# Kernel optimization log

Hardware: AMD Instinct MI355X
Metric: run time of the kernel (lower is better)

Reference implementation:

```python
import jax, jax.numpy as jnp
import numpy as np

T, D, E, K = 8192, 4096, 64, 8


def setup_inputs() -> dict:
    key = jax.random.key(0)
    k1, k2, k3, k4 = jax.random.split(key, 4)
    x = jax.random.normal(k1, (T, D), dtype=jnp.float32)
    # nn.Linear stores weight as [out_features, in_features]
    Wg = jax.random.normal(k2, (E, D), dtype=jnp.float32) * (1.0 / np.sqrt(D))
    Wc = jax.random.normal(k3, (E, D), dtype=jnp.float32) * (1.0 / np.sqrt(D))
    extra_scale = jnp.zeros((E,), dtype=jnp.float32)  # init zeros as in module
    extra_bias = jax.random.normal(k4, (E,), dtype=jnp.float32) * 0.01
    return {"x": x, "Wg": Wg, "Wc": Wc, "extra_scale": extra_scale,
            "extra_bias": extra_bias, "topk": K}


def reference(x, Wg, Wc, extra_scale, extra_bias, topk):
    # scores = |classifier(x) * silu(gate(x))|, softmax in fp32
    gate = jnp.einsum('td,ed->te', x, Wg)        # [T, E]
    cls = jnp.einsum('td,ed->te', x, Wc)         # [T, E]
    scores = jnp.abs(cls * jax.nn.silu(gate))
    scores = jax.nn.softmax(scores.astype(jnp.float32), axis=-1)
    biased = scores + extra_bias[None, :]        # load-balance bias, used only for selection
    _, indices = jax.lax.top_k(biased, topk)     # [T, K]
    original = 1.0 + scores * extra_scale[None, :]
    weights = jnp.take_along_axis(original, indices, axis=1)  # [T, K]
    return weights.astype(x.dtype), indices
```

## Files before the change

### kernel.cpp

```cpp
#include <hip/hip_runtime.h>
#include <math.h>


#define T_DIM 8192
#define D_DIM 4096
#define E_DIM 64
#define N2    128
#define KTOP  8
#define MB_ROWS 128

typedef __attribute__((ext_vector_type(8)))  short bfrag8;
typedef __attribute__((ext_vector_type(16))) float f32x16;

__device__ __forceinline__ unsigned short f2bf_rne(float f) {
    unsigned int u = __float_as_uint(f);
    unsigned int r = u + 0x7fffu + ((u >> 16) & 1u);
    return (unsigned short)(r >> 16);
}
__device__ __forceinline__ float bf2f(unsigned short h) {
    return __uint_as_float(((unsigned int)h) << 16);
}
__device__ __forceinline__ void split3(float v, unsigned short& h,
                                       unsigned short& m, unsigned short& l) {
    h = f2bf_rne(v);
    const float r1 = v - bf2f(h);
    m = f2bf_rne(r1);
    const float r2 = r1 - bf2f(m);
    l = f2bf_rne(r2);
}

__global__ __launch_bounds__(256)
void router_prep(const float* __restrict__ Wg, const float* __restrict__ Wc,
                 unsigned short* __restrict__ Whi, unsigned short* __restrict__ Wmid,
                 unsigned short* __restrict__ Wlo)
{
    const int i   = blockIdx.x * 256 + threadIdx.x;
    const int row = i >> 10;
    const float* src = (row < E_DIM) ? (Wg + (size_t)row * D_DIM)
                                     : (Wc + (size_t)(row - E_DIM) * D_DIM);
    const float4 w = ((const float4*)src)[i & 1023];
    const float v[4] = {w.x, w.y, w.z, w.w};
    ushort4 hv, mv, lv;
    split3(v[0], hv.x, mv.x, lv.x);
    split3(v[1], hv.y, mv.y, lv.y);
    split3(v[2], hv.z, mv.z, lv.z);
    split3(v[3], hv.w, mv.w, lv.w);
    *(ushort4*)(Whi  + (size_t)i * 4) = hv;
    *(ushort4*)(Wmid + (size_t)i * 4) = mv;
    *(ushort4*)(Wlo  + (size_t)i * 4) = lv;
}

__global__ __launch_bounds__(256, 2)
void router_gemm(const float* __restrict__ x,
                 const unsigned short* __restrict__ Whi,
                 const unsigned short* __restrict__ Wmid,
                 const unsigned short* __restrict__ Wlo,
                 float* __restrict__ P,
                 int sliceK)
{
    const int tid  = threadIdx.x;
    const int lane = tid & 63;
    const int wid  = tid >> 6;
    const int l31  = lane & 31;
    const int lh   = lane >> 5;
    const int mb   = blockIdx.x;
    const int ks   = blockIdx.y;
    const int k0   = ks * sliceK;
    const int kend = k0 + sliceK;
    const int row0 = mb * MB_ROWS + wid * 32;

    f32x16 acc[4];
    #pragma unroll
    for (int n = 0; n < 4; ++n)
        #pragma unroll
        for (int r = 0; r < 16; ++r)
            acc[n][r] = 0.f;

    const float* xr = x + (size_t)(row0 + l31) * D_DIM;

    const float* xp0 = xr + k0 + lh * 8;
    float4 a00 = *(const float4*)(xp0);
    float4 a01 = *(const float4*)(xp0 + 4);
    float4 a10 = *(const float4*)(xp0 + 16);
    float4 a11 = *(const float4*)(xp0 + 20);

    for (int kk = k0; kk < kend; kk += 32) {
        bfrag8 ah[2], am[2], al[2];
        {
            const float av0[8] = {a00.x,a00.y,a00.z,a00.w,a01.x,a01.y,a01.z,a01.w};
            const float av1[8] = {a10.x,a10.y,a10.z,a10.w,a11.x,a11.y,a11.z,a11.w};
            #pragma unroll
            for (int j = 0; j < 8; ++j) {
                unsigned short h, m, l;
                split3(av0[j], h, m, l);
                ah[0][j] = (short)h; am[0][j] = (short)m; al[0][j] = (short)l;
                split3(av1[j], h, m, l);
                ah[1][j] = (short)h; am[1][j] = (short)m; al[1][j] = (short)l;
            }
        }

        if (kk + 32 < kend) {
            const float* xp = xr + (kk + 32) + lh * 8;
            a00 = *(const float4*)(xp);
            a01 = *(const float4*)(xp + 4);
            a10 = *(const float4*)(xp + 16);
            a11 = *(const float4*)(xp + 20);
        }

        #pragma unroll
        for (int n = 0; n < 4; ++n) {
            #pragma unroll
            for (int h2 = 0; h2 < 2; ++h2) {
                const size_t bo = (size_t)(n * 32 + l31) * D_DIM + kk + h2 * 16 + lh * 8;
                const bfrag8 bh = *(const bfrag8*)(Whi  + bo);
                const bfrag8 bm = *(const bfrag8*)(Wmid + bo);
                const bfrag8 bl = *(const bfrag8*)(Wlo  + bo);
                acc[n] = __builtin_amdgcn_mfma_f32_32x32x16_bf16(ah[h2], bl, acc[n], 0, 0, 0);
                acc[n] = __builtin_amdgcn_mfma_f32_32x32x16_bf16(al[h2], bh, acc[n], 0, 0, 0);
                acc[n] = __builtin_amdgcn_mfma_f32_32x32x16_bf16(am[h2], bm, acc[n], 0, 0, 0);
                acc[n] = __builtin_amdgcn_mfma_f32_32x32x16_bf16(ah[h2], bm, acc[n], 0, 0, 0);
                acc[n] = __builtin_amdgcn_mfma_f32_32x32x16_bf16(am[h2], bh, acc[n], 0, 0, 0);
                acc[n] = __builtin_amdgcn_mfma_f32_32x32x16_bf16(ah[h2], bh, acc[n], 0, 0, 0);
            }
        }
    }

    float* Pb = P + ((size_t)ks * T_DIM + row0) * N2 + l31;
    #pragma unroll
    for (int n = 0; n < 4; ++n)
        #pragma unroll
        for (int r = 0; r < 16; ++r) {
            const int wrow = (r & 3) + 8 * (r >> 2) + 4 * lh;
            Pb[(size_t)wrow * N2 + n * 32] = acc[n][r];
        }
}

__global__ __launch_bounds__(256)
void router_topk(const float* __restrict__ P,
                 const float* __restrict__ scale,
                 const float* __restrict__ bias,
                 float* __restrict__ out,
                 int ksplit)
{
    const int lane = threadIdx.x & 63;
    const int wid  = threadIdx.x >> 6;
    const int row  = blockIdx.x * 4 + wid;

    float g = 0.f, c = 0.f;
    for (int ks = 0; ks < ksplit; ++ks) {
        const float* p = P + ((size_t)ks * T_DIM + row) * N2;
        g += p[lane];
        c += p[E_DIM + lane];
    }
    const float sg = g / (1.f + expf(-g));
    const float v  = fabsf(c * sg);

    float m = v;
    #pragma unroll
    for (int off = 32; off >= 1; off >>= 1) m = fmaxf(m, __shfl_xor(m, off));
    const float e = expf(v - m);
    float Z = e;
    #pragma unroll
    for (int off = 32; off >= 1; off >>= 1) Z += __shfl_xor(Z, off);
    const float s = e / Z;

    const float sc  = scale[lane];
    float cur = s + bias[lane];

    float myw = 0.f; int myi = 0;
    #pragma unroll
    for (int j = 0; j < KTOP; ++j) {
        float bv = cur; int bi = lane;
        #pragma unroll
        for (int off = 32; off >= 1; off >>= 1) {
            const float ov = __shfl_xor(bv, off);
            const int   oi = __shfl_xor(bi, off);
            if (ov > bv || (ov == bv && oi < bi)) { bv = ov; bi = oi; }
        }
        const float s_bi  = __shfl(s,  bi);
        const float sc_bi = __shfl(sc, bi);
        const float w = 1.f + s_bi * sc_bi;
        if (lane == j)  { myw = w; myi = bi; }
        if (lane == bi) cur = -INFINITY;
    }

    if (lane < KTOP) {
        out[(size_t)row * KTOP + lane] = myw;
        out[(size_t)T_DIM * KTOP + (size_t)row * KTOP + lane] = (float)myi;
    }
}

extern "C" void kernel_launch(void* const* d_in, const int* in_sizes, int n_in,
                              void* d_out, int out_size, void* d_ws, size_t ws_size,
                              hipStream_t stream)
{
    const float* x  = (const float*)d_in[0];
    const float* Wg = (const float*)d_in[1];
    const float* Wc = (const float*)d_in[2];
    const float* sc = (const float*)d_in[3];
    const float* bs = (const float*)d_in[4];
    float* out = (float*)d_out;
    float* P   = (float*)d_ws;

    const size_t PER = (size_t)T_DIM * N2 * sizeof(float);
    const size_t WSP = (size_t)N2 * D_DIM * sizeof(unsigned short);

    int S = 8;
    while (S > 1 && (size_t)S * PER + 3 * WSP > ws_size) S >>= 1;
    const int sliceK = D_DIM / S;

    unsigned short* Whi  = (unsigned short*)((char*)d_ws + (size_t)S * PER);
    unsigned short* Wmid = Whi + (size_t)N2 * D_DIM;
    unsigned short* Wlo  = Wmid + (size_t)N2 * D_DIM;

    router_prep<<<512, 256, 0, stream>>>(Wg, Wc, Whi, Wmid, Wlo);
    router_gemm<<<dim3(T_DIM / MB_ROWS, S), 256, 0, stream>>>(x, Whi, Wmid, Wlo, P, sliceK);
    router_topk<<<T_DIM / 4, 256, 0, stream>>>(P, sc, bs, out, S);
}
```

Baseline: 303.7 us.

## Split GEMM warps 2x2 over rows and columns with double-buffered A/B register prefetch

Changes the block tile from 128 rows with each warp covering all 128 output columns to 64 rows with a 2x2 warp grid, each warp covering 32 rows by 64 columns. This halves the accumulators per warp and doubles the grid size. The K loop is unrolled by two and uses ping-pong register sets, so both the x fragments and the three bf16 weight fragments for the next step are loaded while the current MFMAs run. The goal is to hide global-load latency and raise occupancy. In exchange, each x row is now read by two warps, and the extra prefetch buffers add register pressure.

```diff
diff --git a/kernel.cpp b/kernel.cpp
--- a/kernel.cpp
+++ b/kernel.cpp
@@ -7,7 +7,7 @@
 #define E_DIM 64
 #define N2    128
 #define KTOP  8
-#define MB_ROWS 128
+#define MB_ROWS 64
 
 typedef __attribute__((ext_vector_type(8)))  short bfrag8;
 typedef __attribute__((ext_vector_type(16))) float f32x16;
@@ -50,6 +50,68 @@
     *(ushort4*)(Wlo  + (size_t)i * 4) = lv;
 }
 
+struct ASet { float4 c[4]; };
+struct BSet { bfrag8 h[4], m[4], l[4]; };
+
+__device__ __forceinline__ void loadA(ASet& A, const float* __restrict__ xr, int kk, int lh)
+{
+    const float* p = xr + kk + lh * 8;
+    A.c[0] = *(const float4*)(p);
+    A.c[1] = *(const float4*)(p + 4);
+    A.c[2] = *(const float4*)(p + 16);
+    A.c[3] = *(const float4*)(p + 20);
+}
+
+__device__ __forceinline__ void loadB(BSet& B,
+                                      const unsigned short* __restrict__ Whi,
+                                      const unsigned short* __restrict__ Wmid,
+                                      const unsigned short* __restrict__ Wlo,
+                                      size_t base )
+{
+    #pragma unroll
+    for (int n = 0; n < 2; ++n)
+        #pragma unroll
+        for (int h2 = 0; h2 < 2; ++h2) {
+            const size_t off = base + (size_t)n * 32 * D_DIM + h2 * 16;
+            B.h[n * 2 + h2] = *(const bfrag8*)(Whi  + off);
+            B.m[n * 2 + h2] = *(const bfrag8*)(Wmid + off);
+            B.l[n * 2 + h2] = *(const bfrag8*)(Wlo  + off);
+        }
+}
+
+__device__ __forceinline__ void splitA(const ASet& A, bfrag8 ah[2], bfrag8 am[2], bfrag8 al[2])
+{
+    #pragma unroll
+    for (int h2 = 0; h2 < 2; ++h2) {
+        const float4 q0 = A.c[h2 * 2], q1 = A.c[h2 * 2 + 1];
+        const float f[8] = {q0.x, q0.y, q0.z, q0.w, q1.x, q1.y, q1.z, q1.w};
+        #pragma unroll
+        for (int j = 0; j < 8; ++j) {
+            unsigned short h, m, l;
+            split3(f[j], h, m, l);
+            ah[h2][j] = (short)h; am[h2][j] = (short)m; al[h2][j] = (short)l;
+        }
+    }
+}
+
+__device__ __forceinline__ void mfmaStep(f32x16 acc[2], const bfrag8 ah[2],
+                                         const bfrag8 am[2], const bfrag8 al[2],
+                                         const BSet& B)
+{
+    #pragma unroll
+    for (int n = 0; n < 2; ++n)
+        #pragma unroll
+        for (int h2 = 0; h2 < 2; ++h2) {
+            const int q = n * 2 + h2;
+            acc[n] = __builtin_amdgcn_mfma_f32_32x32x16_bf16(ah[h2], B.l[q], acc[n], 0, 0, 0);
+            acc[n] = __builtin_amdgcn_mfma_f32_32x32x16_bf16(al[h2], B.h[q], acc[n], 0, 0, 0);
+            acc[n] = __builtin_amdgcn_mfma_f32_32x32x16_bf16(am[h2], B.m[q], acc[n], 0, 0, 0);
+            acc[n] = __builtin_amdgcn_mfma_f32_32x32x16_bf16(ah[h2], B.m[q], acc[n], 0, 0, 0);
+            acc[n] = __builtin_amdgcn_mfma_f32_32x32x16_bf16(am[h2], B.h[q], acc[n], 0, 0, 0);
+            acc[n] = __builtin_amdgcn_mfma_f32_32x32x16_bf16(ah[h2], B.h[q], acc[n], 0, 0, 0);
+        }
+}
+
 __global__ __launch_bounds__(256, 2)
 void router_gemm(const float* __restrict__ x,
                  const unsigned short* __restrict__ Whi,
@@ -61,73 +123,53 @@
     const int tid  = threadIdx.x;
     const int lane = tid & 63;
     const int wid  = tid >> 6;
+    const int wr   = wid >> 1;
+    const int wc   = wid & 1;
     const int l31  = lane & 31;
     const int lh   = lane >> 5;
     const int mb   = blockIdx.x;
     const int ks   = blockIdx.y;
     const int k0   = ks * sliceK;
     const int kend = k0 + sliceK;
-    const int row0 = mb * MB_ROWS + wid * 32;
-
-    f32x16 acc[4];
-    #pragma unroll
-    for (int n = 0; n < 4; ++n)
+    const int row0 = mb * MB_ROWS + wr * 32;
+    const int nbase = wc * 64;
+
+    f32x16 acc[2];
+    #pragma unroll
+    for (int n = 0; n < 2; ++n)
         #pragma unroll
         for (int r = 0; r < 16; ++r)
             acc[n][r] = 0.f;
 
     const float* xr = x + (size_t)(row0 + l31) * D_DIM;
-
-    const float* xp0 = xr + k0 + lh * 8;
-    float4 a00 = *(const float4*)(xp0);
-    float4 a01 = *(const float4*)(xp0 + 4);
-    float4 a10 = *(const float4*)(xp0 + 16);
-    float4 a11 = *(const float4*)(xp0 + 20);
-
-    for (int kk = k0; kk < kend; kk += 32) {
-        bfrag8 ah[2], am[2], al[2];
-        {
-            const float av0[8] = {a00.x,a00.y,a00.z,a00.w,a01.x,a01.y,a01.z,a01.w};
-            const float av1[8] = {a10.x,a10.y,a10.z,a10.w,a11.x,a11.y,a11.z,a11.w};
-            #pragma unroll
-            for (int j = 0; j < 8; ++j) {
-                unsigned short h, m, l;
-                split3(av0[j], h, m, l);
-                ah[0][j] = (short)h; am[0][j] = (short)m; al[0][j] = (short)l;
-                split3(av1[j], h, m, l);
-                ah[1][j] = (short)h; am[1][j] = (short)m; al[1][j] = (short)l;
-            }
-        }
-
+    const size_t bbase = (size_t)(nbase + l31) * D_DIM + lh * 8;
+
+    ASet aX, aY;
+    BSet bX, bY;
+    bfrag8 ah[2], am[2], al[2];
+
+    loadA(aX, xr, k0, lh);
+    loadB(bX, Whi, Wmid, Wlo, bbase + k0);
+
+    for (int kk = k0; kk < kend; kk += 64) {
+        splitA(aX, ah, am, al);
         if (kk + 32 < kend) {
-            const float* xp = xr + (kk + 32) + lh * 8;
-            a00 = *(const float4*)(xp);
-            a01 = *(const float4*)(xp + 4);
-            a10 = *(const float4*)(xp + 16);
-            a11 = *(const float4*)(xp + 20);
-        }
-
-        #pragma unroll
-        for (int n = 0; n < 4; ++n) {
-            #pragma unroll
-            for (int h2 = 0; h2 < 2; ++h2) {
-                const size_t bo = (size_t)(n * 32 + l31) * D_DIM + kk + h2 * 16 + lh * 8;
-                const bfrag8 bh = *(const bfrag8*)(Whi  + bo);
-                const bfrag8 bm = *(const bfrag8*)(Wmid + bo);
-                const bfrag8 bl = *(const bfrag8*)(Wlo  + bo);
-                acc[n] = __builtin_amdgcn_mfma_f32_32x32x16_bf16(ah[h2], bl, acc[n], 0, 0, 0);
-                acc[n] = __builtin_amdgcn_mfma_f32_32x32x16_bf16(al[h2], bh, acc[n], 0, 0, 0);
-                acc[n] = __builtin_amdgcn_mfma_f32_32x32x16_bf16(am[h2], bm, acc[n], 0, 0, 0);
-                acc[n] = __builtin_amdgcn_mfma_f32_32x32x16_bf16(ah[h2], bm, acc[n], 0, 0, 0);
-                acc[n] = __builtin_amdgcn_mfma_f32_32x32x16_bf16(am[h2], bh, acc[n], 0, 0, 0);
-                acc[n] = __builtin_amdgcn_mfma_f32_32x32x16_bf16(ah[h2], bh, acc[n], 0, 0, 0);
-            }
-        }
-    }
-
-    float* Pb = P + ((size_t)ks * T_DIM + row0) * N2 + l31;
-    #pragma unroll
-    for (int n = 0; n < 4; ++n)
+            loadA(aY, xr, kk + 32, lh);
+            loadB(bY, Whi, Wmid, Wlo, bbase + kk + 32);
+        }
+        mfmaStep(acc, ah, am, al, bX);
+
+        splitA(aY, ah, am, al);
+        if (kk + 64 < kend) {
+            loadA(aX, xr, kk + 64, lh);
+            loadB(bX, Whi, Wmid, Wlo, bbase + kk + 64);
+        }
+        mfmaStep(acc, ah, am, al, bY);
+    }
+
+    float* Pb = P + ((size_t)ks * T_DIM + row0) * N2 + nbase + l31;
+    #pragma unroll
+    for (int n = 0; n < 2; ++n)
         #pragma unroll
         for (int r = 0; r < 16; ++r) {
             const int wrow = (r & 3) + 8 * (r >> 2) + 4 * lh;
```

Result: slower. 313.0 us (+3.1%).

## Stage x tiles through LDS via async loads and pre-pack W fragments

Applied to the files above, without the earlier changes.

The x operand is now loaded with global_load_lds into a double-buffered, XOR-swizzled shared tile instead of strided per-lane global loads. The prep kernel writes the hi/mid/lo bf16 weight splits in a packed, fragment-ordered layout so each lane's B fragment load is contiguous. This targets the uncoalesced global access pattern of the GEMM. It adds per-tile __syncthreads and LDS usage, which may reduce occupancy or latency hiding.

```diff
diff --git a/kernel.cpp b/kernel.cpp
--- a/kernel.cpp
+++ b/kernel.cpp
@@ -29,35 +29,50 @@
     l = f2bf_rne(r2);
 }
 
+__device__ __forceinline__ void gload16(const void* g, void* l) {
+    __builtin_amdgcn_global_load_lds(
+        (const __attribute__((address_space(1))) void*)g,
+        (__attribute__((address_space(3))) void*)l, 16, 0, 0);
+}
+
 __global__ __launch_bounds__(256)
 void router_prep(const float* __restrict__ Wg, const float* __restrict__ Wc,
-                 unsigned short* __restrict__ Whi, unsigned short* __restrict__ Wmid,
-                 unsigned short* __restrict__ Wlo)
-{
-    const int i   = blockIdx.x * 256 + threadIdx.x;
-    const int row = i >> 10;
-    const float* src = (row < E_DIM) ? (Wg + (size_t)row * D_DIM)
-                                     : (Wc + (size_t)(row - E_DIM) * D_DIM);
-    const float4 w = ((const float4*)src)[i & 1023];
-    const float v[4] = {w.x, w.y, w.z, w.w};
-    ushort4 hv, mv, lv;
-    split3(v[0], hv.x, mv.x, lv.x);
-    split3(v[1], hv.y, mv.y, lv.y);
-    split3(v[2], hv.z, mv.z, lv.z);
-    split3(v[3], hv.w, mv.w, lv.w);
-    *(ushort4*)(Whi  + (size_t)i * 4) = hv;
-    *(ushort4*)(Wmid + (size_t)i * 4) = mv;
-    *(ushort4*)(Wlo  + (size_t)i * 4) = lv;
+                 unsigned short* __restrict__ Wpk)
+{
+    const int t   = blockIdx.x * 256 + threadIdx.x;
+    const int col = t >> 9;
+    const int ch  = t & 511;
+    const int k   = ch << 3;
+
+    const float* src = (col < E_DIM) ? (Wg + (size_t)col * D_DIM)
+                                     : (Wc + (size_t)(col - E_DIM) * D_DIM);
+    const float4 w0 = ((const float4*)(src + k))[0];
+    const float4 w1 = ((const float4*)(src + k))[1];
+    const float v[8] = {w0.x, w0.y, w0.z, w0.w, w1.x, w1.y, w1.z, w1.w};
+
+    unsigned short hv[8], mv[8], lv[8];
+    #pragma unroll
+    for (int j = 0; j < 8; ++j) split3(v[j], hv[j], mv[j], lv[j]);
+
+    const int k32 = k >> 5, h2 = (k >> 4) & 1, lh = (k >> 3) & 1;
+    const int n = col >> 5, lane = lh * 32 + (col & 31);
+    const size_t base = ((((size_t)k32 * 4 + n) * 3 + 0) * 2 + h2) * 512 + (size_t)lane * 8;
+    *(ushort4*)(Wpk + base)          = make_ushort4(hv[0], hv[1], hv[2], hv[3]);
+    *(ushort4*)(Wpk + base + 4)      = make_ushort4(hv[4], hv[5], hv[6], hv[7]);
+    *(ushort4*)(Wpk + base + 1024)   = make_ushort4(mv[0], mv[1], mv[2], mv[3]);
+    *(ushort4*)(Wpk + base + 1028)   = make_ushort4(mv[4], mv[5], mv[6], mv[7]);
+    *(ushort4*)(Wpk + base + 2048)   = make_ushort4(lv[0], lv[1], lv[2], lv[3]);
+    *(ushort4*)(Wpk + base + 2052)   = make_ushort4(lv[4], lv[5], lv[6], lv[7]);
 }
 
 __global__ __launch_bounds__(256, 2)
 void router_gemm(const float* __restrict__ x,
-                 const unsigned short* __restrict__ Whi,
-                 const unsigned short* __restrict__ Wmid,
-                 const unsigned short* __restrict__ Wlo,
+                 const unsigned short* __restrict__ Wpk,
                  float* __restrict__ P,
                  int sliceK)
 {
+    __shared__ float sA[2][MB_ROWS * 32];
+
     const int tid  = threadIdx.x;
     const int lane = tid & 63;
     const int wid  = tid >> 6;
@@ -66,8 +81,10 @@
     const int mb   = blockIdx.x;
     const int ks   = blockIdx.y;
     const int k0   = ks * sliceK;
-    const int kend = k0 + sliceK;
-    const int row0 = mb * MB_ROWS + wid * 32;
+    const int NT   = sliceK >> 5;
+    const int brow0 = mb * MB_ROWS;
+    const int rl   = wid * 32 + l31;
+    const int sw   = l31 & 7;
 
     f32x16 acc[4];
     #pragma unroll
@@ -76,45 +93,53 @@
         for (int r = 0; r < 16; ++r)
             acc[n][r] = 0.f;
 
-    const float* xr = x + (size_t)(row0 + l31) * D_DIM;
-
-    const float* xp0 = xr + k0 + lh * 8;
-    float4 a00 = *(const float4*)(xp0);
-    float4 a01 = *(const float4*)(xp0 + 4);
-    float4 a10 = *(const float4*)(xp0 + 16);
-    float4 a11 = *(const float4*)(xp0 + 20);
-
-    for (int kk = k0; kk < kend; kk += 32) {
+    #define STAGE(bf_, kk_)                                                      \
+        {                                                                        \
+            _Pragma("unroll")                                                    \
+            for (int i_ = 0; i_ < 4; ++i_) {                                     \
+                const int chunk_ = i_ * 256 + tid;                               \
+                const int row_   = chunk_ >> 3;                                  \
+                const int csrc_  = (chunk_ & 7) ^ (row_ & 7);                    \
+                const float* gp_ = x + (size_t)(brow0 + row_) * D_DIM            \
+                                     + (kk_) + csrc_ * 4;                        \
+                gload16(gp_, &sA[bf_][chunk_ * 4]);                              \
+            }                                                                    \
+        }
+
+    STAGE(0, k0);
+    __syncthreads();
+
+    for (int t = 0; t < NT; ++t) {
+        const int kk = k0 + t * 32;
+        const int bf = t & 1;
+
+        if (t + 1 < NT) STAGE(bf ^ 1, kk + 32);
+
         bfrag8 ah[2], am[2], al[2];
-        {
-            const float av0[8] = {a00.x,a00.y,a00.z,a00.w,a01.x,a01.y,a01.z,a01.w};
-            const float av1[8] = {a10.x,a10.y,a10.z,a10.w,a11.x,a11.y,a11.z,a11.w};
+        #pragma unroll
+        for (int h2 = 0; h2 < 2; ++h2) {
+            const int c0 = h2 * 4 + lh * 2;
+            const float4 q0 = *(const float4*)&sA[bf][rl * 32 + ((c0    ) ^ sw) * 4];
+            const float4 q1 = *(const float4*)&sA[bf][rl * 32 + ((c0 + 1) ^ sw) * 4];
+            const float f[8] = {q0.x, q0.y, q0.z, q0.w, q1.x, q1.y, q1.z, q1.w};
             #pragma unroll
             for (int j = 0; j < 8; ++j) {
                 unsigned short h, m, l;
-                split3(av0[j], h, m, l);
-                ah[0][j] = (short)h; am[0][j] = (short)m; al[0][j] = (short)l;
-                split3(av1[j], h, m, l);
-                ah[1][j] = (short)h; am[1][j] = (short)m; al[1][j] = (short)l;
+                split3(f[j], h, m, l);
+                ah[h2][j] = (short)h; am[h2][j] = (short)m; al[h2][j] = (short)l;
             }
         }
 
-        if (kk + 32 < kend) {
-            const float* xp = xr + (kk + 32) + lh * 8;
-            a00 = *(const float4*)(xp);
-            a01 = *(const float4*)(xp + 4);
-            a10 = *(const float4*)(xp + 16);
-            a11 = *(const float4*)(xp + 20);
-        }
-
+        const size_t k32 = (size_t)(kk >> 5);
         #pragma unroll
         for (int n = 0; n < 4; ++n) {
             #pragma unroll
             for (int h2 = 0; h2 < 2; ++h2) {
-                const size_t bo = (size_t)(n * 32 + l31) * D_DIM + kk + h2 * 16 + lh * 8;
-                const bfrag8 bh = *(const bfrag8*)(Whi  + bo);
-                const bfrag8 bm = *(const bfrag8*)(Wmid + bo);
-                const bfrag8 bl = *(const bfrag8*)(Wlo  + bo);
+                const unsigned short* bb =
+                    Wpk + ((((k32 * 4 + n) * 3 + 0) * 2 + h2) * 64 + lane) * 8;
+                const bfrag8 bh = *(const bfrag8*)(bb);
+                const bfrag8 bm = *(const bfrag8*)(bb + 1024);
+                const bfrag8 bl = *(const bfrag8*)(bb + 2048);
                 acc[n] = __builtin_amdgcn_mfma_f32_32x32x16_bf16(ah[h2], bl, acc[n], 0, 0, 0);
                 acc[n] = __builtin_amdgcn_mfma_f32_32x32x16_bf16(al[h2], bh, acc[n], 0, 0, 0);
                 acc[n] = __builtin_amdgcn_mfma_f32_32x32x16_bf16(am[h2], bm, acc[n], 0, 0, 0);
@@ -123,9 +148,11 @@
                 acc[n] = __builtin_amdgcn_mfma_f32_32x32x16_bf16(ah[h2], bh, acc[n], 0, 0, 0);
             }
         }
-    }
-
-    float* Pb = P + ((size_t)ks * T_DIM + row0) * N2 + l31;
+
+        __syncthreads();
+    }
+
+    float* Pb = P + ((size_t)ks * T_DIM + brow0 + wid * 32) * N2 + l31;
     #pragma unroll
     for (int n = 0; n < 4; ++n)
         #pragma unroll
@@ -209,11 +236,9 @@
     while (S > 1 && (size_t)S * PER + 3 * WSP > ws_size) S >>= 1;
     const int sliceK = D_DIM / S;
 
-    unsigned short* Whi  = (unsigned short*)((char*)d_ws + (size_t)S * PER);
-    unsigned short* Wmid = Whi + (size_t)N2 * D_DIM;
-    unsigned short* Wlo  = Wmid + (size_t)N2 * D_DIM;
-
-    router_prep<<<512, 256, 0, stream>>>(Wg, Wc, Whi, Wmid, Wlo);
-    router_gemm<<<dim3(T_DIM / MB_ROWS, S), 256, 0, stream>>>(x, Whi, Wmid, Wlo, P, sliceK);
+    unsigned short* Wpk = (unsigned short*)((char*)d_ws + (size_t)S * PER);
+
+    router_prep<<<256, 256, 0, stream>>>(Wg, Wc, Wpk);
+    router_gemm<<<dim3(T_DIM / MB_ROWS, S), 256, 0, stream>>>(x, Wpk, P, sliceK);
     router_topk<<<T_DIM / 4, 256, 0, stream>>>(P, sc, bs, out, S);
 }
```

Measured after the change: 298.4 us. No clear change (-1.7%).
